# Performance work log

Hardware: AMD Instinct MI355X
Metric: run time of the kernel (lower is better)

## Reference

```python
import jax, jax.numpy as jnp
import numpy as np

B, DIM, H, W = 8, 512, 32, 32
NUM_HEADS, KEY_DIM, VALUE_DIM, DIM_OUT = 8, 64, 64, 512


def setup_inputs() -> dict:
    key = jax.random.key(0)
    ks = jax.random.split(key, 5)
    return {
        "x": jax.random.normal(ks[0], (B, DIM, H, W), dtype=jnp.float32),
        "query_proj": jax.random.normal(ks[1], (NUM_HEADS, KEY_DIM, DIM), dtype=jnp.float32),
        "key_proj": jax.random.normal(ks[2], (DIM, KEY_DIM), dtype=jnp.float32),
        "value_proj": jax.random.normal(ks[3], (DIM, VALUE_DIM), dtype=jnp.float32),
        "out_proj": jax.random.normal(ks[4], (DIM_OUT, NUM_HEADS, VALUE_DIM), dtype=jnp.float32),
    }


def reference(x, query_proj, key_proj, value_proj, out_proj):
    b, d, h, w = x.shape
    key_dim = query_proj.shape[1]
    scale = key_dim ** (-0.5)
    # flatten spatial dims to tokens: [b, n, d] where n = h*w (m == x here)
    rx = jnp.transpose(x.reshape(b, d, h * w), (0, 2, 1))
    q = jnp.einsum('bnd,hkd->bnhk', rx, query_proj)
    k = jnp.einsum('bmd,dk->bmk', rx, key_proj)          # single shared K head
    attn = jax.nn.softmax(jnp.einsum('bnhk,bmk->bnhm', q, k) * scale, axis=-1)
    v = jnp.einsum('bmd,dv->bmv', rx, value_proj)        # single shared V head
    o = jnp.einsum('bnhm,bmv->bnhv', attn, v)
    result = jnp.einsum('bnhv,dhv->bdn', o, out_proj)
    return result.reshape(b, -1, h, w)
```

## Files before the change

### kernel.cpp

```cpp
#include <hip/hip_runtime.h>
#include <math.h>

#define BATCH 8
#define DIMD  512
#define NTOK  1024
#define NH    8
#define CQKV  640
#define DOUT  512

typedef __attribute__((ext_vector_type(8))) short short8;
typedef __attribute__((ext_vector_type(4))) short short4v;
typedef __attribute__((ext_vector_type(4))) float f32x4;

__device__ __forceinline__ short bf16rn(float x) {
    unsigned u = __float_as_uint(x);
    u += 0x7FFF + ((u >> 16) & 1);
    return (short)(u >> 16);
}
__device__ __forceinline__ float bf16tof(short s) {
    return __uint_as_float(((unsigned)(unsigned short)s) << 16);
}
struct HL { short h, l; };
__device__ __forceinline__ HL bf16split(float x) {
    HL r;
    r.h = bf16rn(x);
    r.l = bf16rn(x - bf16tof(r.h));
    return r;
}
__device__ __forceinline__ void dma16(const short* g, short* l) {
    __builtin_amdgcn_global_load_lds(
        (const __attribute__((address_space(1))) unsigned int*)g,
        (__attribute__((address_space(3))) unsigned int*)l, 16, 0, 0);
}
__device__ __forceinline__ float swzmax16(float v) {
    v = fmaxf(v, __int_as_float(__builtin_amdgcn_ds_swizzle(__float_as_int(v), 0x041F)));
    v = fmaxf(v, __int_as_float(__builtin_amdgcn_ds_swizzle(__float_as_int(v), 0x081F)));
    v = fmaxf(v, __int_as_float(__builtin_amdgcn_ds_swizzle(__float_as_int(v), 0x101F)));
    v = fmaxf(v, __int_as_float(__builtin_amdgcn_ds_swizzle(__float_as_int(v), 0x201F)));
    return v;
}
__device__ __forceinline__ unsigned packbf2(float f0, float f1) {
    return __builtin_amdgcn_perm(__float_as_uint(f1), __float_as_uint(f0), 0x07060302);
}


__global__ __launch_bounds__(256) void prepack_all(const float* __restrict__ x,
                                                   const float* __restrict__ qp,
                                                   const float* __restrict__ kp,
                                                   const float* __restrict__ vp,
                                                   const float* __restrict__ wout,
                                                   short* __restrict__ whi,
                                                   short* __restrict__ wlo,
                                                   short* __restrict__ xhi,
                                                   short* __restrict__ xlo,
                                                   short* __restrict__ wof) {
    __shared__ float Cs[64][65];
    const int blk = blockIdx.x;
    const int t = threadIdx.x;
    if (blk < 1024) {
        const int nt = blk & 15, dt = (blk >> 4) & 7, b = blk >> 7;
        #pragma unroll
        for (int i = 0; i < 4; ++i) {
            int row = (t >> 4) + i * 16;
            float4 v = *(const float4*)(x + ((size_t)(b * DIMD + dt * 64 + row)) * NTOK
                                          + nt * 64 + (t & 15) * 4);
            Cs[row][(t & 15) * 4 + 0] = v.x;
            Cs[row][(t & 15) * 4 + 1] = v.y;
            Cs[row][(t & 15) * 4 + 2] = v.z;
            Cs[row][(t & 15) * 4 + 3] = v.w;
        }
        __syncthreads();
        for (int u = t; u < 512; u += 256) {
            int lane2 = u & 63, cidx = u >> 6;
            int q2 = lane2 >> 4, r2 = lane2 & 15;
            int kt_loc = cidx & 1, mt_loc = cidx >> 1;
            short8 h8, l8;
            #pragma unroll
            for (int j = 0; j < 8; ++j) {
                HL s = bf16split(Cs[kt_loc * 32 + q2 * 8 + j][mt_loc * 16 + r2]);
                h8[j] = s.h; l8[j] = s.l;
            }
            size_t off = (((size_t)(b * 64 + nt * 4 + mt_loc)) * 16 + dt * 2 + kt_loc) * 512
                         + lane2 * 8;
            *(short8*)&xhi[off] = h8;
            *(short8*)&xlo[off] = l8;
        }
    } else if (blk < 1184) {
        int tid = (blk - 1024) * 256 + t;
        int lane = tid & 63, kt = (tid >> 6) & 15, ct = tid >> 10;
        int q = lane >> 4, r = lane & 15;
        int c = ct * 16 + r;
        short8 h, l;
        #pragma unroll
        for (int j = 0; j < 8; ++j) {
            int d = kt * 32 + q * 8 + j;
            float v;
            if (c < 64)       v = kp[d * 64 + c];
            else if (c < 128) v = vp[d * 64 + (c - 64)];
            else              v = qp[(size_t)(c - 128) * DIMD + d];
            HL s = bf16split(v);
            h[j] = s.h; l[j] = s.l;
        }
        *(short8*)&whi[(size_t)tid * 8] = h;
        *(short8*)&wlo[(size_t)tid * 8] = l;
    } else {
        int tid = (blk - 1184) * 256 + t;
        int lane = tid & 63, kt = (tid >> 6) & 15, mt = tid >> 10;
        int q = lane >> 4, r = lane & 15;
        const float* src = wout + (size_t)(mt * 16 + r) * DOUT + kt * 32 + q * 8;
        short8 h;
        #pragma unroll
        for (int j = 0; j < 8; ++j) h[j] = bf16rn(src[j]);
        *(short8*)&wof[(size_t)tid * 8] = h;
    }
}

__global__ __launch_bounds__(256) void qkv_gemm(const short* __restrict__ xhi,
                                                const short* __restrict__ xlo,
                                                const short* __restrict__ whi,
                                                const short* __restrict__ wlo,
                                                short* __restrict__ khi,
                                                short* __restrict__ klo,
                                                short* __restrict__ vf,
                                                short* __restrict__ qhi,
                                                short* __restrict__ qlo) {
    __shared__ __align__(16) char pool[49152];
    short* Ah = (short*)pool;
    short* Al = Ah + 8192;
    short* Bh = Al + 8192;
    short* Bl = Bh + 4096;
    float (*Cs)[65] = (float(*)[65])pool;

    const int idx = blockIdx.x;
    const int low = idx & 7, rest = idx >> 3;
    const int cb = rest % 10, gh = rest / 10;
    const int g = gh * 8 + low;
    const int b = g >> 3, bml = g & 7;

    const int tid = threadIdx.x, w = tid >> 6, lane = tid & 63;
    const int q = lane >> 4, r = lane & 15;
    f32x4 acc[2][4];
    #pragma unroll
    for (int i = 0; i < 2; ++i)
        #pragma unroll
        for (int j = 0; j < 4; ++j) acc[i][j] = (f32x4){0.f, 0.f, 0.f, 0.f};

    for (int it = 0; it < 8; ++it) {
        __syncthreads();
        for (int u = w; u < 16; u += 4) {
            size_t ga = ((size_t)((b * 64 + bml * 8 + (u >> 1)) * 16 + it * 2 + (u & 1))) * 512 + lane * 8;
            dma16(xhi + ga, &Ah[u * 512]);
            dma16(xlo + ga, &Al[u * 512]);
            if (u < 8) {
                size_t gb = ((size_t)((cb * 4 + (u >> 1)) * 16 + it * 2 + (u & 1))) * 512 + lane * 8;
                dma16(whi + gb, &Bh[u * 512]);
                dma16(wlo + gb, &Bl[u * 512]);
            }
        }
        __syncthreads();
        #pragma unroll
        for (int kc = 0; kc < 2; ++kc) {
            short8 ah[2], al[2];
            #pragma unroll
            for (int rt = 0; rt < 2; ++rt) {
                ah[rt] = *(short8*)&Ah[((w * 2 + rt) * 2 + kc) * 512 + lane * 8];
                al[rt] = *(short8*)&Al[((w * 2 + rt) * 2 + kc) * 512 + lane * 8];
            }
            #pragma unroll
            for (int tt = 0; tt < 4; ++tt) {
                short8 bh = *(short8*)&Bh[(tt * 2 + kc) * 512 + lane * 8];
                short8 bl = *(short8*)&Bl[(tt * 2 + kc) * 512 + lane * 8];
                #pragma unroll
                for (int rt = 0; rt < 2; ++rt) {
                    acc[rt][tt] = __builtin_amdgcn_mfma_f32_16x16x32_bf16(ah[rt], bh, acc[rt][tt], 0, 0, 0);
                    acc[rt][tt] = __builtin_amdgcn_mfma_f32_16x16x32_bf16(ah[rt], bl, acc[rt][tt], 0, 0, 0);
                    acc[rt][tt] = __builtin_amdgcn_mfma_f32_16x16x32_bf16(al[rt], bh, acc[rt][tt], 0, 0, 0);
                }
            }
        }
    }

    __syncthreads();
    #pragma unroll
    for (int rt = 0; rt < 2; ++rt)
        #pragma unroll
        for (int reg = 0; reg < 4; ++reg)
            #pragma unroll
            for (int tt = 0; tt < 4; ++tt)
                Cs[w * 32 + rt * 16 + q * 4 + reg][tt * 16 + r] = acc[rt][tt][reg];
    __syncthreads();

    if (cb == 0) {
        for (int u = tid; u < 1024; u += 256) {
            int lane2 = u & 63, ic = (u >> 6) & 7, tl = u >> 9;
            int q2 = lane2 >> 4, r2 = lane2 & 15;
            int i = ic >> 1, cc = ic & 1;
            short8 h8, l8;
            #pragma unroll
            for (int j = 0; j < 8; ++j) {
                HL s = bf16split(Cs[tl * 64 + i * 16 + r2][cc * 32 + q2 * 8 + j]);
                h8[j] = s.h; l8[j] = s.l;
            }
            size_t off = ((size_t)(b * 16 + bml * 2 + tl) * 8 + ic) * 512 + lane2 * 8;
            *(short8*)&khi[off] = h8;
            *(short8*)&klo[off] = l8;
        }
    } else if (cb == 1) {
        for (int u = tid; u < 1024; u += 256) {
            int lane2 = u & 63, ic = (u >> 6) & 7, tl = u >> 9;
            int q2 = lane2 >> 4, r2 = lane2 & 15;
            int tv = ic >> 1, cc = ic & 1;
            short8 v8;
            #pragma unroll
            for (int j = 0; j < 8; ++j)
                v8[j] = bf16rn(Cs[tl * 64 + cc * 32 + q2 * 8 + j][tv * 16 + r2]);
            size_t off = ((size_t)(b * 16 + bml * 2 + tl) * 8 + ic) * 512 + lane2 * 8;
            *(short8*)&vf[off] = v8;
        }
    } else {
        const int hd = cb - 2;
        const float qscale = 0.125f * 1.44269504f;
        for (int u = tid; u < 1024; u += 256) {
            int lane2 = u & 63, ch = u >> 6;
            int q2 = lane2 >> 4, r2 = lane2 & 15;
            int kc = ch & 1, ntl = ch >> 1;
            short8 h8, l8;
            #pragma unroll
            for (int j = 0; j < 8; ++j) {
                HL s = bf16split(Cs[ntl * 16 + r2][kc * 32 + q2 * 8 + j] * qscale);
                h8[j] = s.h; l8[j] = s.l;
            }
            size_t off = ((((size_t)(b * 8 + hd) * 64 + bml * 8 + ntl) * 2 + kc) * 64 + lane2) * 8;
            *(short8*)&qhi[off] = h8;
            *(short8*)&qlo[off] = l8;
        }
    }
}

__global__ __launch_bounds__(256) void attn_mfma(const short* __restrict__ qhi_g,
                                                 const short* __restrict__ qlo_g,
                                                 const short* __restrict__ khi_g,
                                                 const short* __restrict__ klo_g,
                                                 const short* __restrict__ vf_g,
                                                 short* __restrict__ ob) {
    __shared__ short Khi[4096], Klo[4096], Vf[4096];
    __shared__ short Pbuf[4 * 64 * 36];
    const int blk = blockIdx.x;
    const int b   = blk & 7;
    const int h   = (blk >> 3) & 7;
    const int qt  = blk >> 6;
    const int tid = threadIdx.x;
    const int w    = tid >> 6;
    const int lane = tid & 63;
    const int q    = lane >> 4;
    const int r    = lane & 15;
    short* Pw = Pbuf + w * (64 * 36);

    short8 qhi[2][2], qlo[2][2];
    #pragma unroll
    for (int rt = 0; rt < 2; ++rt) {
        const int nt = qt * 8 + w * 2 + rt;
        #pragma unroll
        for (int c = 0; c < 2; ++c) {
            size_t off = ((((size_t)(b * 8 + h) * 64 + nt) * 2 + c) * 64 + lane) * 8;
            qhi[rt][c] = *(const short8*)&qhi_g[off];
            qlo[rt][c] = *(const short8*)&qlo_g[off];
        }
    }

    short8 bones;
    #pragma unroll
    for (int j = 0; j < 8; ++j) bones[j] = (short)0x3F80;

    f32x4 oacc[2][4], lacc[2];
    float m_[2][4];
    #pragma unroll
    for (int rt = 0; rt < 2; ++rt) {
        #pragma unroll
        for (int tt = 0; tt < 4; ++tt) oacc[rt][tt] = (f32x4){0.f, 0.f, 0.f, 0.f};
        lacc[rt] = (f32x4){0.f, 0.f, 0.f, 0.f};
        #pragma unroll
        for (int i = 0; i < 4; ++i) m_[rt][i] = -1e30f;
    }

    for (int t = 0; t < 16; ++t) {
        __syncthreads();
        const size_t kb = ((size_t)(b * 16 + t) * 8) * 512;
        for (int ch = w; ch < 8; ch += 4) {
            dma16(khi_g + kb + ch * 512 + lane * 8, &Khi[ch * 512]);
            dma16(klo_g + kb + ch * 512 + lane * 8, &Klo[ch * 512]);
            dma16(vf_g  + kb + ch * 512 + lane * 8, &Vf [ch * 512]);
        }
        __syncthreads();

        f32x4 s[2][4];
        #pragma unroll
        for (int rt = 0; rt < 2; ++rt)
            #pragma unroll
            for (int tt = 0; tt < 4; ++tt) s[rt][tt] = (f32x4){0.f, 0.f, 0.f, 0.f};
        #pragma unroll
        for (int c = 0; c < 2; ++c) {
            #pragma unroll
            for (int tt = 0; tt < 4; ++tt) {
                short8 kh = *(short8*)&Khi[((tt * 2 + c) * 64 + lane) * 8];
                short8 kl = *(short8*)&Klo[((tt * 2 + c) * 64 + lane) * 8];
                #pragma unroll
                for (int rt = 0; rt < 2; ++rt) {
                    s[rt][tt] = __builtin_amdgcn_mfma_f32_16x16x32_bf16(qhi[rt][c], kh, s[rt][tt], 0, 0, 0);
                    s[rt][tt] = __builtin_amdgcn_mfma_f32_16x16x32_bf16(qhi[rt][c], kl, s[rt][tt], 0, 0, 0);
                    s[rt][tt] = __builtin_amdgcn_mfma_f32_16x16x32_bf16(qlo[rt][c], kh, s[rt][tt], 0, 0, 0);
                }
            }
        }

        float pmax[2][4];
        bool need = false;
        #pragma unroll
        for (int rt = 0; rt < 2; ++rt)
            #pragma unroll
            for (int reg = 0; reg < 4; ++reg) {
                float pm = fmaxf(fmaxf(s[rt][0][reg], s[rt][1][reg]),
                                 fmaxf(s[rt][2][reg], s[rt][3][reg]));
                pmax[rt][reg] = pm;
                need = need || (pm > m_[rt][reg] + 30.f);
            }
        if (__any((int)need)) {
            #pragma unroll
            for (int rt = 0; rt < 2; ++rt)
                #pragma unroll
                for (int reg = 0; reg < 4; ++reg) {
                    float smax = swzmax16(pmax[rt][reg]);
                    float nm    = fmaxf(m_[rt][reg], smax);
                    float alpha = exp2f(m_[rt][reg] - nm);
                    m_[rt][reg] = nm;
                    lacc[rt][reg] *= alpha;
                    #pragma unroll
                    for (int tt = 0; tt < 4; ++tt) oacc[rt][tt][reg] *= alpha;
                }
        }
        #pragma unroll
        for (int rt = 0; rt < 2; ++rt)
            #pragma unroll
            for (int reg = 0; reg < 4; ++reg)
                #pragma unroll
                for (int tt = 0; tt < 4; ++tt)
                    s[rt][tt][reg] = exp2f(s[rt][tt][reg] - m_[rt][reg]);

        #pragma unroll
        for (int rt = 0; rt < 2; ++rt) {
            #pragma unroll
            for (int tt = 0; tt < 4; ++tt) {
                uint2 pk;
                pk.x = packbf2(s[rt][tt][0], s[rt][tt][1]);
                pk.y = packbf2(s[rt][tt][2], s[rt][tt][3]);
                *(uint2*)&Pw[(r + 16 * tt) * 36 + rt * 16 + q * 4] = pk;
            }
        }

        #pragma unroll
        for (int c = 0; c < 2; ++c) {
            short8 pf[2];
            #pragma unroll
            for (int rt = 0; rt < 2; ++rt)
                #pragma unroll
                for (int j = 0; j < 8; ++j)
                    pf[rt][j] = Pw[(c * 32 + q * 8 + j) * 36 + rt * 16 + r];
            #pragma unroll
            for (int rt = 0; rt < 2; ++rt)
                lacc[rt] = __builtin_amdgcn_mfma_f32_16x16x32_bf16(pf[rt], bones, lacc[rt], 0, 0, 0);
            #pragma unroll
            for (int tt = 0; tt < 4; ++tt) {
                short8 vfr = *(short8*)&Vf[((tt * 2 + c) * 64 + lane) * 8];
                #pragma unroll
                for (int rt = 0; rt < 2; ++rt)
                    oacc[rt][tt] = __builtin_amdgcn_mfma_f32_16x16x32_bf16(pf[rt], vfr, oacc[rt][tt], 0, 0, 0);
            }
        }
    }

    #pragma unroll
    for (int rt = 0; rt < 2; ++rt) {
        const int nt = qt * 8 + w * 2 + rt;
        #pragma unroll
        for (int reg = 0; reg < 4; ++reg) {
            float inv = 1.f / lacc[rt][reg];
            #pragma unroll
            for (int tt = 0; tt < 4; ++tt) {
                int ct = h * 2 + (tt >> 1);
                int lanep = ((tt & 1) * 2 + (r >> 3)) * 16 + q * 4 + reg;
                ob[((((size_t)b * 64 + nt) * 16 + ct) * 64 + lanep) * 8 + (r & 7)] =
                    bf16rn(oacc[rt][tt][reg] * inv);
            }
        }
    }
}

__global__ __launch_bounds__(256) void out_gemm(const short* __restrict__ wof,
                                                const short* __restrict__ obf,
                                                float* __restrict__ out) {
    __shared__ short Ah[2][4096];
    __shared__ short Bh[2][4096];
    const int b = blockIdx.z, bd = blockIdx.y, bn = blockIdx.x;
    const int tid = threadIdx.x, w = tid >> 6, lane = tid & 63;
    const int q = lane >> 4, r = lane & 15;
    f32x4 acc[4];
    #pragma unroll
    for (int j = 0; j < 4; ++j) acc[j] = (f32x4){0.f, 0.f, 0.f, 0.f};

    for (int u = w; u < 8; u += 4) {
        size_t ga = ((size_t)((bd * 4 + (u >> 1)) * 16 + (u & 1))) * 512 + lane * 8;
        dma16(wof + ga, &Ah[0][u * 512]);
        size_t gb = ((size_t)((b * 64 + bn * 4 + (u >> 1)) * 16 + (u & 1))) * 512 + lane * 8;
        dma16(obf + gb, &Bh[0][u * 512]);
    }

    for (int it = 0; it < 8; ++it) {
        const int cur = it & 1;
        __syncthreads();
        if (it < 7) {
            for (int u = w; u < 8; u += 4) {
                size_t ga = ((size_t)((bd * 4 + (u >> 1)) * 16 + (it + 1) * 2 + (u & 1))) * 512 + lane * 8;
                dma16(wof + ga, &Ah[cur ^ 1][u * 512]);
                size_t gb = ((size_t)((b * 64 + bn * 4 + (u >> 1)) * 16 + (it + 1) * 2 + (u & 1))) * 512 + lane * 8;
                dma16(obf + gb, &Bh[cur ^ 1][u * 512]);
            }
        }
        #pragma unroll
        for (int kc = 0; kc < 2; ++kc) {
            short8 a = *(short8*)&Ah[cur][(w * 2 + kc) * 512 + lane * 8];
            #pragma unroll
            for (int tt = 0; tt < 4; ++tt) {
                short8 bb = *(short8*)&Bh[cur][(tt * 2 + kc) * 512 + lane * 8];
                acc[tt] = __builtin_amdgcn_mfma_f32_16x16x32_bf16(a, bb, acc[tt], 0, 0, 0);
            }
        }
    }
    const int d_base = bd * 64 + w * 16;
    #pragma unroll
    for (int reg = 0; reg < 4; ++reg)
        #pragma unroll
        for (int tt = 0; tt < 4; ++tt)
            out[((size_t)b * DOUT + d_base + q * 4 + reg) * NTOK
                + bn * 64 + tt * 16 + r] = acc[tt][reg];
}

extern "C" void kernel_launch(void* const* d_in, const int* in_sizes, int n_in,
                              void* d_out, int out_size, void* d_ws, size_t ws_size,
                              hipStream_t stream) {
    const float* x  = (const float*)d_in[0];
    const float* qp = (const float*)d_in[1];
    const float* kp = (const float*)d_in[2];
    const float* vp = (const float*)d_in[3];
    const float* op = (const float*)d_in[4];
    float* out = (float*)d_out;

    short* Whi = (short*)d_ws;
    short* Wlo = Whi + 327680;
    short* Xhi = Wlo + 327680;
    short* Xlo = Xhi + 4194304;
    short* Qhi = Xlo + 4194304;
    short* Qlo = Qhi + 4194304;
    short* Khi = Qlo + 4194304;
    short* Klo = Khi + 524288;
    short* Vf  = Klo + 524288;
    short* Wof = Vf  + 524288;
    short* Ob  = Xhi;

    prepack_all <<<1312, 256, 0, stream>>>(x, qp, kp, vp, op,
                                           Whi, Wlo, Xhi, Xlo, Wof);
    qkv_gemm    <<<640, 256, 0, stream>>>(Xhi, Xlo, Whi, Wlo,
                                          Khi, Klo, Vf, Qhi, Qlo);
    attn_mfma   <<<512, 256, 0, stream>>>(Qhi, Qlo, Khi, Klo, Vf, Ob);
    out_gemm    <<<dim3(16, 8, BATCH), 256, 0, stream>>>(Wof, Ob, out);
}
```

Before: 170.5 us.

## Double-buffer K/V tiles and use 8 waves with one query tile each

The attention kernel now runs 512 threads per block, with each of the 8 waves owning a single 16-row query tile instead of two. K/V tiles are double-buffered in shared memory, and the next tile is prefetched by async DMA while the current one is computed, which removes one barrier per iteration. This targets the serialized load/compute pattern and raises waves per block. In exchange, each wave does half the MFMA work per K/V load, so register reuse of K/V fragments drops, and shared memory doubles for the K/V buffers.

```diff
diff --git a/kernel.cpp b/kernel.cpp
--- a/kernel.cpp
+++ b/kernel.cpp
@@ -237,14 +237,14 @@
     }
 }
 
-__global__ __launch_bounds__(256) void attn_mfma(const short* __restrict__ qhi_g,
+__global__ __launch_bounds__(512) void attn_mfma(const short* __restrict__ qhi_g,
                                                  const short* __restrict__ qlo_g,
                                                  const short* __restrict__ khi_g,
                                                  const short* __restrict__ klo_g,
                                                  const short* __restrict__ vf_g,
                                                  short* __restrict__ ob) {
-    __shared__ short Khi[4096], Klo[4096], Vf[4096];
-    __shared__ short Pbuf[4 * 64 * 36];
+    __shared__ short Khi[2][4096], Klo[2][4096], Vf[2][4096];
+    __shared__ short Pbuf[8 * 64 * 20];
     const int blk = blockIdx.x;
     const int b   = blk & 7;
     const int h   = (blk >> 3) & 7;
@@ -254,143 +254,122 @@
     const int lane = tid & 63;
     const int q    = lane >> 4;
     const int r    = lane & 15;
-    short* Pw = Pbuf + w * (64 * 36);
-
-    short8 qhi[2][2], qlo[2][2];
-    #pragma unroll
-    for (int rt = 0; rt < 2; ++rt) {
-        const int nt = qt * 8 + w * 2 + rt;
+    short* Pw = Pbuf + w * (64 * 20);
+    const int nt = qt * 8 + w;
+
+    short8 qhi[2], qlo[2];
+    #pragma unroll
+    for (int c = 0; c < 2; ++c) {
+        size_t off = ((((size_t)(b * 8 + h) * 64 + nt) * 2 + c) * 64 + lane) * 8;
+        qhi[c] = *(const short8*)&qhi_g[off];
+        qlo[c] = *(const short8*)&qlo_g[off];
+    }
+
+    short8 bones;
+    #pragma unroll
+    for (int j = 0; j < 8; ++j) bones[j] = (short)0x3F80;
+
+    f32x4 oacc[4], lacc;
+    float m_[4];
+    #pragma unroll
+    for (int tt = 0; tt < 4; ++tt) oacc[tt] = (f32x4){0.f, 0.f, 0.f, 0.f};
+    lacc = (f32x4){0.f, 0.f, 0.f, 0.f};
+    #pragma unroll
+    for (int i = 0; i < 4; ++i) m_[i] = -1e30f;
+
+    {
+        const size_t kb = ((size_t)(b * 16 + 0) * 8) * 512;
+        dma16(khi_g + kb + w * 512 + lane * 8, &Khi[0][w * 512]);
+        dma16(klo_g + kb + w * 512 + lane * 8, &Klo[0][w * 512]);
+        dma16(vf_g  + kb + w * 512 + lane * 8, &Vf [0][w * 512]);
+    }
+
+    for (int t = 0; t < 16; ++t) {
+        const int cur = t & 1;
+        __builtin_amdgcn_sched_barrier(0);
+        asm volatile("s_waitcnt vmcnt(0) lgkmcnt(0)" ::: "memory");
+        __builtin_amdgcn_sched_barrier(0);
+        __syncthreads();
+        if (t < 15) {
+            const size_t kb = ((size_t)(b * 16 + t + 1) * 8) * 512;
+            dma16(khi_g + kb + w * 512 + lane * 8, &Khi[cur ^ 1][w * 512]);
+            dma16(klo_g + kb + w * 512 + lane * 8, &Klo[cur ^ 1][w * 512]);
+            dma16(vf_g  + kb + w * 512 + lane * 8, &Vf [cur ^ 1][w * 512]);
+        }
+
+        f32x4 s[4];
+        #pragma unroll
+        for (int tt = 0; tt < 4; ++tt) s[tt] = (f32x4){0.f, 0.f, 0.f, 0.f};
         #pragma unroll
         for (int c = 0; c < 2; ++c) {
-            size_t off = ((((size_t)(b * 8 + h) * 64 + nt) * 2 + c) * 64 + lane) * 8;
-            qhi[rt][c] = *(const short8*)&qhi_g[off];
-            qlo[rt][c] = *(const short8*)&qlo_g[off];
-        }
-    }
-
-    short8 bones;
-    #pragma unroll
-    for (int j = 0; j < 8; ++j) bones[j] = (short)0x3F80;
-
-    f32x4 oacc[2][4], lacc[2];
-    float m_[2][4];
-    #pragma unroll
-    for (int rt = 0; rt < 2; ++rt) {
-        #pragma unroll
-        for (int tt = 0; tt < 4; ++tt) oacc[rt][tt] = (f32x4){0.f, 0.f, 0.f, 0.f};
-        lacc[rt] = (f32x4){0.f, 0.f, 0.f, 0.f};
-        #pragma unroll
-        for (int i = 0; i < 4; ++i) m_[rt][i] = -1e30f;
-    }
-
-    for (int t = 0; t < 16; ++t) {
-        __syncthreads();
-        const size_t kb = ((size_t)(b * 16 + t) * 8) * 512;
-        for (int ch = w; ch < 8; ch += 4) {
-            dma16(khi_g + kb + ch * 512 + lane * 8, &Khi[ch * 512]);
-            dma16(klo_g + kb + ch * 512 + lane * 8, &Klo[ch * 512]);
-            dma16(vf_g  + kb + ch * 512 + lane * 8, &Vf [ch * 512]);
-        }
-        __syncthreads();
-
-        f32x4 s[2][4];
-        #pragma unroll
-        for (int rt = 0; rt < 2; ++rt)
-            #pragma unroll
-            for (int tt = 0; tt < 4; ++tt) s[rt][tt] = (f32x4){0.f, 0.f, 0.f, 0.f};
+            #pragma unroll
+            for (int tt = 0; tt < 4; ++tt) {
+                short8 kh = *(short8*)&Khi[cur][((tt * 2 + c) * 64 + lane) * 8];
+                short8 kl = *(short8*)&Klo[cur][((tt * 2 + c) * 64 + lane) * 8];
+                s[tt] = __builtin_amdgcn_mfma_f32_16x16x32_bf16(qhi[c], kh, s[tt], 0, 0, 0);
+                s[tt] = __builtin_amdgcn_mfma_f32_16x16x32_bf16(qhi[c], kl, s[tt], 0, 0, 0);
+                s[tt] = __builtin_amdgcn_mfma_f32_16x16x32_bf16(qlo[c], kh, s[tt], 0, 0, 0);
+            }
+        }
+
+        float pmax[4];
+        bool need = false;
+        #pragma unroll
+        for (int reg = 0; reg < 4; ++reg) {
+            float pm = fmaxf(fmaxf(s[0][reg], s[1][reg]), fmaxf(s[2][reg], s[3][reg]));
+            pmax[reg] = pm;
+            need = need || (pm > m_[reg] + 30.f);
+        }
+        if (__any((int)need)) {
+            #pragma unroll
+            for (int reg = 0; reg < 4; ++reg) {
+                float smax = swzmax16(pmax[reg]);
+                float nm    = fmaxf(m_[reg], smax);
+                float alpha = exp2f(m_[reg] - nm);
+                m_[reg] = nm;
+                lacc[reg] *= alpha;
+                #pragma unroll
+                for (int tt = 0; tt < 4; ++tt) oacc[tt][reg] *= alpha;
+            }
+        }
+        #pragma unroll
+        for (int reg = 0; reg < 4; ++reg)
+            #pragma unroll
+            for (int tt = 0; tt < 4; ++tt)
+                s[tt][reg] = exp2f(s[tt][reg] - m_[reg]);
+
+        #pragma unroll
+        for (int tt = 0; tt < 4; ++tt) {
+            uint2 pk;
+            pk.x = packbf2(s[tt][0], s[tt][1]);
+            pk.y = packbf2(s[tt][2], s[tt][3]);
+            *(uint2*)&Pw[(r + 16 * tt) * 20 + q * 4] = pk;
+        }
+
         #pragma unroll
         for (int c = 0; c < 2; ++c) {
+            short8 pf;
+            #pragma unroll
+            for (int j = 0; j < 8; ++j)
+                pf[j] = Pw[(c * 32 + q * 8 + j) * 20 + r];
+            lacc = __builtin_amdgcn_mfma_f32_16x16x32_bf16(pf, bones, lacc, 0, 0, 0);
             #pragma unroll
             for (int tt = 0; tt < 4; ++tt) {
-                short8 kh = *(short8*)&Khi[((tt * 2 + c) * 64 + lane) * 8];
-                short8 kl = *(short8*)&Klo[((tt * 2 + c) * 64 + lane) * 8];
-                #pragma unroll
-                for (int rt = 0; rt < 2; ++rt) {
-                    s[rt][tt] = __builtin_amdgcn_mfma_f32_16x16x32_bf16(qhi[rt][c], kh, s[rt][tt], 0, 0, 0);
-                    s[rt][tt] = __builtin_amdgcn_mfma_f32_16x16x32_bf16(qhi[rt][c], kl, s[rt][tt], 0, 0, 0);
-                    s[rt][tt] = __builtin_amdgcn_mfma_f32_16x16x32_bf16(qlo[rt][c], kh, s[rt][tt], 0, 0, 0);
-                }
-            }
-        }
-
-        float pmax[2][4];
-        bool need = false;
-        #pragma unroll
-        for (int rt = 0; rt < 2; ++rt)
-            #pragma unroll
-            for (int reg = 0; reg < 4; ++reg) {
-                float pm = fmaxf(fmaxf(s[rt][0][reg], s[rt][1][reg]),
-                                 fmaxf(s[rt][2][reg], s[rt][3][reg]));
-                pmax[rt][reg] = pm;
-                need = need || (pm > m_[rt][reg] + 30.f);
-            }
-        if (__any((int)need)) {
-            #pragma unroll
-            for (int rt = 0; rt < 2; ++rt)
-                #pragma unroll
-                for (int reg = 0; reg < 4; ++reg) {
-                    float smax = swzmax16(pmax[rt][reg]);
-                    float nm    = fmaxf(m_[rt][reg], smax);
-                    float alpha = exp2f(m_[rt][reg] - nm);
-                    m_[rt][reg] = nm;
-                    lacc[rt][reg] *= alpha;
-                    #pragma unroll
-                    for (int tt = 0; tt < 4; ++tt) oacc[rt][tt][reg] *= alpha;
-                }
-        }
-        #pragma unroll
-        for (int rt = 0; rt < 2; ++rt)
-            #pragma unroll
-            for (int reg = 0; reg < 4; ++reg)
-                #pragma unroll
-                for (int tt = 0; tt < 4; ++tt)
-                    s[rt][tt][reg] = exp2f(s[rt][tt][reg] - m_[rt][reg]);
-
-        #pragma unroll
-        for (int rt = 0; rt < 2; ++rt) {
-            #pragma unroll
-            for (int tt = 0; tt < 4; ++tt) {
-                uint2 pk;
-                pk.x = packbf2(s[rt][tt][0], s[rt][tt][1]);
-                pk.y = packbf2(s[rt][tt][2], s[rt][tt][3]);
-                *(uint2*)&Pw[(r + 16 * tt) * 36 + rt * 16 + q * 4] = pk;
-            }
-        }
-
-        #pragma unroll
-        for (int c = 0; c < 2; ++c) {
-            short8 pf[2];
-            #pragma unroll
-            for (int rt = 0; rt < 2; ++rt)
-                #pragma unroll
-                for (int j = 0; j < 8; ++j)
-                    pf[rt][j] = Pw[(c * 32 + q * 8 + j) * 36 + rt * 16 + r];
-            #pragma unroll
-            for (int rt = 0; rt < 2; ++rt)
-                lacc[rt] = __builtin_amdgcn_mfma_f32_16x16x32_bf16(pf[rt], bones, lacc[rt], 0, 0, 0);
-            #pragma unroll
-            for (int tt = 0; tt < 4; ++tt) {
-                short8 vfr = *(short8*)&Vf[((tt * 2 + c) * 64 + lane) * 8];
-                #pragma unroll
-                for (int rt = 0; rt < 2; ++rt)
-                    oacc[rt][tt] = __builtin_amdgcn_mfma_f32_16x16x32_bf16(pf[rt], vfr, oacc[rt][tt], 0, 0, 0);
-            }
-        }
-    }
-
-    #pragma unroll
-    for (int rt = 0; rt < 2; ++rt) {
-        const int nt = qt * 8 + w * 2 + rt;
-        #pragma unroll
-        for (int reg = 0; reg < 4; ++reg) {
-            float inv = 1.f / lacc[rt][reg];
-            #pragma unroll
-            for (int tt = 0; tt < 4; ++tt) {
-                int ct = h * 2 + (tt >> 1);
-                int lanep = ((tt & 1) * 2 + (r >> 3)) * 16 + q * 4 + reg;
-                ob[((((size_t)b * 64 + nt) * 16 + ct) * 64 + lanep) * 8 + (r & 7)] =
-                    bf16rn(oacc[rt][tt][reg] * inv);
-            }
+                short8 vfr = *(short8*)&Vf[cur][((tt * 2 + c) * 64 + lane) * 8];
+                oacc[tt] = __builtin_amdgcn_mfma_f32_16x16x32_bf16(pf, vfr, oacc[tt], 0, 0, 0);
+            }
+        }
+    }
+
+    #pragma unroll
+    for (int reg = 0; reg < 4; ++reg) {
+        float inv = 1.f / lacc[reg];
+        #pragma unroll
+        for (int tt = 0; tt < 4; ++tt) {
+            int ct = h * 2 + (tt >> 1);
+            int lanep = ((tt & 1) * 2 + (r >> 3)) * 16 + q * 4 + reg;
+            ob[((((size_t)b * 64 + nt) * 16 + ct) * 64 + lanep) * 8 + (r & 7)] =
+                bf16rn(oacc[tt][reg] * inv);
         }
     }
 }
@@ -470,6 +449,6 @@
                                            Whi, Wlo, Xhi, Xlo, Wof);
     qkv_gemm    <<<640, 256, 0, stream>>>(Xhi, Xlo, Whi, Wlo,
                                           Khi, Klo, Vf, Qhi, Qlo);
-    attn_mfma   <<<512, 256, 0, stream>>>(Qhi, Qlo, Khi, Klo, Vf, Ob);
+    attn_mfma   <<<512, 512, 0, stream>>>(Qhi, Qlo, Khi, Klo, Vf, Ob);
     out_gemm    <<<dim3(16, 8, BATCH), 256, 0, stream>>>(Wof, Ob, out);
 }
```

After: 158.3 us. 1.08x faster.
